# Kernel optimization log

Hardware: AMD Instinct MI355X
Metric: run time of the kernel (lower is better)

Reference implementation:

```python
import jax, jax.numpy as jnp
import numpy as np

BATCH = 512
NUM_CLASSES = 100000
MARGIN = 0.5
SCALE = 64.0


def setup_inputs() -> dict:
    key = jax.random.key(0)
    k1, k2 = jax.random.split(key)
    # cosine similarities must lie in [-1, 1] for acos; keep away from the
    # endpoints so acos gradients stay finite.
    costh = jax.random.uniform(k1, (BATCH, NUM_CLASSES), dtype=jnp.float32,
                               minval=-0.99, maxval=0.99)
    label = jax.random.randint(k2, (BATCH,), 0, NUM_CLASSES, dtype=jnp.int64)
    return {"costh": costh, "label": label}


def reference(costh, label):
    # delt_theta = margin * one_hot(label); theta + delt_theta only changes the
    # target-class column, so apply cos(acos(c_y) + margin) at label positions
    # instead of materializing the full one-hot / acos matrices.
    b = costh.shape[0]
    rows = jnp.arange(b)
    c_y = costh[rows, label]                       # (B,)
    c_y_m = jnp.cos(jnp.arccos(c_y) + MARGIN)      # target-class margin shift
    logits = (SCALE * costh).at[rows, label].set(SCALE * c_y_m)  # (B, C)
    # mean cross-entropy
    lse = jax.nn.logsumexp(logits, axis=1)         # (B,)
    loss = jnp.mean(lse - logits[rows, label])
    return loss
```

## Files before the change

kernel.cpp:

```cpp
#include <hip/hip_runtime.h>
#include <hip/hip_bf16.h>

#define BATCH 512
#define NUM_CLASSES 100000
#define NVEC (NUM_CLASSES / 4)
#define BLOCK 512

#define COS_M 0.8775825618903728f
#define SIN_M 0.479425538604203f
#define SHIFT 64.0f

__device__ __forceinline__ float block_reduce_sum(float v) {
    #pragma unroll
    for (int off = 32; off > 0; off >>= 1)
        v += __shfl_down(v, off, 64);
    __shared__ float smem[BLOCK / 64];
    const int lane = threadIdx.x & 63;
    const int wid  = threadIdx.x >> 6;
    if (lane == 0) smem[wid] = v;
    __syncthreads();
    if (wid == 0) {
        v = (lane < (BLOCK / 64)) ? smem[lane] : 0.0f;
        #pragma unroll
        for (int off = 4; off > 0; off >>= 1)
            v += __shfl_down(v, off, 64);
    }
    return v;
}

__global__ __launch_bounds__(BLOCK)
void arc_row_lse(const float* __restrict__ costh,
                 const int*   __restrict__ label,
                 float*       __restrict__ partial) {
    const int row = blockIdx.x;
    const float* rp = costh + (size_t)row * NUM_CLASSES;
    const float4* vp = (const float4*)rp;

    float sum = 0.0f;
    for (int i = threadIdx.x; i < NVEC; i += BLOCK) {
        float4 v = vp[i];
        sum += __expf(fmaf(64.0f, v.x, -SHIFT));
        sum += __expf(fmaf(64.0f, v.y, -SHIFT));
        sum += __expf(fmaf(64.0f, v.z, -SHIFT));
        sum += __expf(fmaf(64.0f, v.w, -SHIFT));
    }

    float tot = block_reduce_sum(sum);

    if (threadIdx.x == 0) {
        const int lab = label[row];
        const float c_y = rp[lab];
        const float t = 64.0f * (c_y * COS_M -
                                 sqrtf(fmaxf(0.0f, 1.0f - c_y * c_y)) * SIN_M);
        const float s = tot - __expf(fmaf(64.0f, c_y, -SHIFT)) + __expf(t - SHIFT);
        partial[row] = (SHIFT + logf(s)) - t;
    }
}

__global__ __launch_bounds__(BLOCK)
void arc_final_reduce(const float* __restrict__ partial,
                      float*       __restrict__ out) {
    float v = partial[threadIdx.x];
    float tot = block_reduce_sum(v);
    if (threadIdx.x == 0)
        out[0] = tot * (1.0f / (float)BATCH);
}

extern "C" void kernel_launch(void* const* d_in, const int* in_sizes, int n_in,
                              void* d_out, int out_size, void* d_ws, size_t ws_size,
                              hipStream_t stream) {
    const float* costh = (const float*)d_in[0];
    const int*   label = (const int*)d_in[1];
    float* out = (float*)d_out;
    float* partial = (float*)d_ws;

    arc_row_lse<<<BATCH, BLOCK, 0, stream>>>(costh, label, partial);
    arc_final_reduce<<<1, BLOCK, 0, stream>>>(partial, out);
}
```

Baseline: 280.8 us.

## Split each row across four blocks and move label correction into final kernel

Each row's exp-sum is now split into four chunks handled by separate 256-thread blocks (2048 blocks instead of 512), which spreads the row work over more blocks to improve occupancy and memory-level parallelism on the many CUs. The inner loop is unrolled twice with two independent accumulators to expose more outstanding loads. The label margin correction and log are moved into the single-block final kernel, one thread per row, which adds a scattered gather there but keeps the streaming kernel simpler.

```diff
diff --git a/kernel.cpp b/kernel.cpp
--- a/kernel.cpp
+++ b/kernel.cpp
@@ -1,69 +1,92 @@
 #include <hip/hip_runtime.h>
-#include <hip/hip_bf16.h>
 
 #define BATCH 512
 #define NUM_CLASSES 100000
 #define NVEC (NUM_CLASSES / 4)
-#define BLOCK 512
+#define CHUNKS 4
+#define CVEC (NVEC / CHUNKS)
+#define BLOCK 256
+#define FBLOCK 512
 
 #define COS_M 0.8775825618903728f
 #define SIN_M 0.479425538604203f
 #define SHIFT 64.0f
 
-__device__ __forceinline__ float block_reduce_sum(float v) {
+__device__ __forceinline__ float wave_reduce(float v) {
     #pragma unroll
     for (int off = 32; off > 0; off >>= 1)
         v += __shfl_down(v, off, 64);
+    return v;
+}
+
+__global__ __launch_bounds__(BLOCK)
+void arc_chunk_sum(const float* __restrict__ costh,
+                   float*       __restrict__ partial) {
+    const int row   = blockIdx.x >> 2;
+    const int chunk = blockIdx.x & (CHUNKS - 1);
+    const float4* vp = (const float4*)(costh + (size_t)row * NUM_CLASSES)
+                       + chunk * CVEC;
+
+    float s0 = 0.0f, s1 = 0.0f;
+    int i = threadIdx.x;
+    for (; i + BLOCK < CVEC; i += 2 * BLOCK) {
+        float4 a = vp[i];
+        float4 b = vp[i + BLOCK];
+        s0 += __expf(fmaf(64.0f, a.x, -SHIFT));
+        s1 += __expf(fmaf(64.0f, a.y, -SHIFT));
+        s0 += __expf(fmaf(64.0f, a.z, -SHIFT));
+        s1 += __expf(fmaf(64.0f, a.w, -SHIFT));
+        s0 += __expf(fmaf(64.0f, b.x, -SHIFT));
+        s1 += __expf(fmaf(64.0f, b.y, -SHIFT));
+        s0 += __expf(fmaf(64.0f, b.z, -SHIFT));
+        s1 += __expf(fmaf(64.0f, b.w, -SHIFT));
+    }
+    if (i < CVEC) {
+        float4 a = vp[i];
+        s0 += __expf(fmaf(64.0f, a.x, -SHIFT));
+        s1 += __expf(fmaf(64.0f, a.y, -SHIFT));
+        s0 += __expf(fmaf(64.0f, a.z, -SHIFT));
+        s1 += __expf(fmaf(64.0f, a.w, -SHIFT));
+    }
+
+    float v = wave_reduce(s0 + s1);
     __shared__ float smem[BLOCK / 64];
     const int lane = threadIdx.x & 63;
     const int wid  = threadIdx.x >> 6;
     if (lane == 0) smem[wid] = v;
     __syncthreads();
-    if (wid == 0) {
-        v = (lane < (BLOCK / 64)) ? smem[lane] : 0.0f;
-        #pragma unroll
-        for (int off = 4; off > 0; off >>= 1)
-            v += __shfl_down(v, off, 64);
-    }
-    return v;
+    if (threadIdx.x == 0)
+        partial[blockIdx.x] = (smem[0] + smem[1]) + (smem[2] + smem[3]);
 }
 
-__global__ __launch_bounds__(BLOCK)
-void arc_row_lse(const float* __restrict__ costh,
-                 const int*   __restrict__ label,
-                 float*       __restrict__ partial) {
-    const int row = blockIdx.x;
-    const float* rp = costh + (size_t)row * NUM_CLASSES;
-    const float4* vp = (const float4*)rp;
+__global__ __launch_bounds__(FBLOCK)
+void arc_final(const float* __restrict__ costh,
+               const int*   __restrict__ label,
+               const float* __restrict__ partial,
+               float*       __restrict__ out) {
+    const int r = threadIdx.x;
+    const float4 p = ((const float4*)partial)[r];
+    const int lab = label[r];
+    const float c_y = costh[(size_t)r * NUM_CLASSES + lab];
 
-    float sum = 0.0f;
-    for (int i = threadIdx.x; i < NVEC; i += BLOCK) {
-        float4 v = vp[i];
-        sum += __expf(fmaf(64.0f, v.x, -SHIFT));
-        sum += __expf(fmaf(64.0f, v.y, -SHIFT));
-        sum += __expf(fmaf(64.0f, v.z, -SHIFT));
-        sum += __expf(fmaf(64.0f, v.w, -SHIFT));
+    float tot = (p.x + p.y) + (p.z + p.w);
+    const float t = 64.0f * (c_y * COS_M -
+                             sqrtf(fmaxf(0.0f, 1.0f - c_y * c_y)) * SIN_M);
+    const float s = tot - __expf(fmaf(64.0f, c_y, -SHIFT)) + __expf(t - SHIFT);
+    float v = (SHIFT + logf(s)) - t;
+
+    v = wave_reduce(v);
+    __shared__ float smem[FBLOCK / 64];
+    const int lane = threadIdx.x & 63;
+    const int wid  = threadIdx.x >> 6;
+    if (lane == 0) smem[wid] = v;
+    __syncthreads();
+    if (threadIdx.x == 0) {
+        float tv = 0.0f;
+        #pragma unroll
+        for (int w = 0; w < FBLOCK / 64; ++w) tv += smem[w];
+        out[0] = tv * (1.0f / (float)BATCH);
     }
-
-    float tot = block_reduce_sum(sum);
-
-    if (threadIdx.x == 0) {
-        const int lab = label[row];
-        const float c_y = rp[lab];
-        const float t = 64.0f * (c_y * COS_M -
-                                 sqrtf(fmaxf(0.0f, 1.0f - c_y * c_y)) * SIN_M);
-        const float s = tot - __expf(fmaf(64.0f, c_y, -SHIFT)) + __expf(t - SHIFT);
-        partial[row] = (SHIFT + logf(s)) - t;
-    }
-}
-
-__global__ __launch_bounds__(BLOCK)
-void arc_final_reduce(const float* __restrict__ partial,
-                      float*       __restrict__ out) {
-    float v = partial[threadIdx.x];
-    float tot = block_reduce_sum(v);
-    if (threadIdx.x == 0)
-        out[0] = tot * (1.0f / (float)BATCH);
 }
 
 extern "C" void kernel_launch(void* const* d_in, const int* in_sizes, int n_in,
@@ -74,6 +97,6 @@
     float* out = (float*)d_out;
     float* partial = (float*)d_ws;
 
-    arc_row_lse<<<BATCH, BLOCK, 0, stream>>>(costh, label, partial);
-    arc_final_reduce<<<1, BLOCK, 0, stream>>>(partial, out);
+    arc_chunk_sum<<<BATCH * CHUNKS, BLOCK, 0, stream>>>(costh, partial);
+    arc_final<<<1, FBLOCK, 0, stream>>>(costh, label, partial, out);
 }
```

After: 282.9 us. About the same (+0.7%).
